# Kernel optimization log

Hardware: AMD Instinct MI355X
Metric: run time of the kernel (lower is better)

Reference implementation:

```python
import math
import jax, jax.numpy as jnp
import numpy as np

CT = {"SDD": 1000.0, "SCD": 500.0, "det_interval": 1.0, "num_det": 736}


def ramp_filter_np(ct, scale):
    # Standard equiangular fan-beam ramp filter (utility.ramp_filter):
    #   h[0] = 1/(8*db^2); h[n odd] = -1/(2*(pi*sin(n*db))^2); h[n even!=0] = 0
    db = ct["det_interval"] / ct["SDD"] * scale  # angular detector pitch at this scale
    n_det = int(ct["num_det"] // scale)
    n = np.arange(-(n_det - 1), n_det)  # length K = 2*n_det - 1
    h = np.zeros(n.shape, dtype=np.float32)
    h[n == 0] = 1.0 / (8.0 * db ** 2)
    odd = (n % 2) != 0
    h[odd] = -0.5 / (np.pi * np.sin(n[odd] * db)) ** 2
    return h


def setup_inputs() -> dict:
    key = jax.random.key(0)
    scale = 1
    batch, ch, view, det = 16, 1, 1152, CT["num_det"] // scale
    sinogram = jax.random.normal(key, (batch, ch, view, det), dtype=jnp.float32)
    delta_b = CT["det_interval"] / CT["SDD"]
    # recon_filter = ramp_filter * scale * delta_b, shaped [1,1,1,K] (OIHW)
    filt = ramp_filter_np(CT, scale) * scale * delta_b
    recon_filter = jnp.asarray(filt, dtype=jnp.float32)[None, None, None, :]
    return {"sinogram": sinogram, "recon_filter": recon_filter, "scale": scale}


def reference(sinogram, recon_filter, scale):
    det = sinogram.shape[-1]
    # cosine fan-beam pre-weighting
    s_range = (CT["det_interval"]
               * jnp.linspace((1.0 - det) / 2.0, (det - 1.0) / 2.0, det, dtype=jnp.float32)
               * scale) / CT["SDD"]
    cos_weight = (CT["SCD"] / 10000.0) * jnp.cos(s_range)  # [det]
    x = sinogram * cos_weight[None, None, None, :]
    # 1D ramp-filter convolution along detector axis (F.conv2d with 1xK kernel)
    K = recon_filter.shape[-1]
    pad = K // 2
    out = jax.lax.conv_general_dilated(
        x, recon_filter,
        window_strides=(1, 1),
        padding=[(0, 0), (pad, pad)],
        dimension_numbers=("NCHW", "OIHW", "NCHW"),
    )
    return out
```

## Files before the change

### kernel.cpp

```cpp
#include <hip/hip_runtime.h>

typedef unsigned short ushort_t;
typedef ushort_t u16x8 __attribute__((ext_vector_type(8)));
typedef __bf16 bf16x8 __attribute__((ext_vector_type(8)));
typedef float f32x4 __attribute__((ext_vector_type(4)));

#define DET 736
#define HALF 368
#define HK 384
#define NTT 12
#define CPB2 (NTT * 64)
#define NRB 1152


__global__ void prep_af(const float* __restrict__ sino,
                        ushort_t* __restrict__ Ae, ushort_t* __restrict__ Ao) {
    int c = blockIdx.x * blockDim.x + threadIdx.x;
    int rblk = c / CPB2;
    int rem  = c - rblk * CPB2;
    int t = rem >> 6, lane = rem & 63;
    int rr = lane & 15, quad = lane >> 4;
    int j0 = t * 32 + quad * 8;
    u16x8 ve, vo;
    if (j0 < HALF) {
        const float* g = sino + (size_t)(rblk * 16 + rr) * DET + 2 * j0;
        float w[16];
        *(f32x4*)(w)      = *(const f32x4*)(g);
        *(f32x4*)(w + 4)  = *(const f32x4*)(g + 4);
        *(f32x4*)(w + 8)  = *(const f32x4*)(g + 8);
        *(f32x4*)(w + 12) = *(const f32x4*)(g + 12);
#pragma unroll
        for (int e = 0; e < 8; ++e) {
            vo[e] = __builtin_bit_cast(ushort_t, (__bf16)w[2 * e]);
            ve[e] = __builtin_bit_cast(ushort_t, (__bf16)w[2 * e + 1]);
        }
    } else {
#pragma unroll
        for (int e = 0; e < 8; ++e) { ve[e] = 0; vo[e] = 0; }
    }
    *(u16x8*)(Ae + (size_t)c * 8) = ve;
    *(u16x8*)(Ao + (size_t)c * 8) = vo;
}

__global__ void prep_bf(const float* __restrict__ filt,
                        ushort_t* __restrict__ Be, ushort_t* __restrict__ Bo) {
    int c = blockIdx.x * blockDim.x + threadIdx.x;
    int cb  = c / CPB2;
    int rem = c - cb * CPB2;
    int t = rem >> 6, lane = rem & 63;
    int i = cb * 16 + (lane & 15);
    int quad = lane >> 4;
    u16x8 ve, vo;
#pragma unroll
    for (int e = 0; e < 8; ++e) {
        int j = t * 32 + quad * 8 + e;
        bool real = (j < HALF) && (i < HALF);
        int de = 2 * (j - i) + 1 + 735;
        int do_ = de - 2;
        de  = de  < 0 ? 0 : (de  > 1470 ? 1470 : de);
        do_ = do_ < 0 ? 0 : (do_ > 1470 ? 1470 : do_);
        float ge = 0.05f * cosf(((float)(2 * j + 1) - 367.5f) * 0.001f);
        float go = 0.05f * cosf(((float)(2 * j)     - 367.5f) * 0.001f);
        float fe = filt[de] * ge;
        float fo = filt[do_] * go;
        ve[e] = real ? __builtin_bit_cast(ushort_t, (__bf16)fe) : (ushort_t)0;
        vo[e] = real ? __builtin_bit_cast(ushort_t, (__bf16)fo) : (ushort_t)0;
    }
    *(u16x8*)(Be + (size_t)c * 8) = ve;
    *(u16x8*)(Bo + (size_t)c * 8) = vo;
}

__global__ __launch_bounds__(1024, 4) void gemm_half(
    const ushort_t* __restrict__ Ae, const ushort_t* __restrict__ Ao,
    const ushort_t* __restrict__ Be, const ushort_t* __restrict__ Bo,
    const float* __restrict__ sino, const float* __restrict__ filt,
    float* __restrict__ C)
{
    __shared__ ushort_t Bs[8 * CPB2 * 8];

    const int p    = blockIdx.z;
    const ushort_t* Af = p ? Ao : Ae;
    const ushort_t* Bf = p ? Bo : Be;

    const int tid  = threadIdx.x;
    const int lane = tid & 63;
    const int wid  = tid >> 6;
    const int wm   = wid >> 1;
    const int wn   = wid & 1;
    const int quad = lane >> 4;
    const int l16  = lane & 15;

    const int cbg0 = blockIdx.y * 8;
    {
        const ushort_t* bsrc = Bf + (size_t)cbg0 * CPB2 * 8;
        for (int c = tid; c < 8 * CPB2; c += 1024)
            *(u16x8*)(Bs + c * 8) = *(const u16x8*)(bsrc + (size_t)c * 8);
    }
    __syncthreads();

    const int rblk0 = blockIdx.x * 32 + wm * 4;

    f32x4 acc[4][4];
#pragma unroll
    for (int i = 0; i < 4; ++i)
#pragma unroll
        for (int j = 0; j < 4; ++j)
            acc[i][j] = (f32x4){0.f, 0.f, 0.f, 0.f};

    const ushort_t* pA[4];
#pragma unroll
    for (int mi = 0; mi < 4; ++mi)
        pA[mi] = Af + ((size_t)(rblk0 + mi) * CPB2 + lane) * 8;
    const ushort_t* pB[4];
#pragma unroll
    for (int ni = 0; ni < 4; ++ni)
        pB[ni] = Bs + ((wn * 4 + ni) * CPB2 + lane) * 8;

    u16x8 acur[4];
#pragma unroll
    for (int mi = 0; mi < 4; ++mi)
        acur[mi] = *(const u16x8*)(pA[mi]);

    for (int t = 0; t < NTT; ++t) {
        u16x8 anx[4];
        if (t + 1 < NTT) {
#pragma unroll
            for (int mi = 0; mi < 4; ++mi)
                anx[mi] = *(const u16x8*)(pA[mi] + (t + 1) * 512);
        }
        u16x8 b[4];
#pragma unroll
        for (int ni = 0; ni < 4; ++ni)
            b[ni] = *(const u16x8*)(pB[ni] + t * 512);
#pragma unroll
        for (int mi = 0; mi < 4; ++mi)
#pragma unroll
            for (int ni = 0; ni < 4; ++ni)
                acc[mi][ni] = __builtin_amdgcn_mfma_f32_16x16x32_bf16(
                    __builtin_bit_cast(bf16x8, acur[mi]),
                    __builtin_bit_cast(bf16x8, b[ni]),
                    acc[mi][ni], 0, 0, 0);
        if (t + 1 < NTT) {
#pragma unroll
            for (int mi = 0; mi < 4; ++mi) acur[mi] = anx[mi];
        }
    }

    const float h0 = filt[735];
    float gwv[4];
    int   ncol[4];
#pragma unroll
    for (int ni = 0; ni < 4; ++ni) {
        int ic   = blockIdx.y * 128 + (wn * 4 + ni) * 16 + l16;
        ncol[ni] = 2 * ic + p;
        gwv[ni]  = h0 * 0.05f * cosf(((float)ncol[ni] - 367.5f) * 0.001f);
    }
#pragma unroll
    for (int mi = 0; mi < 4; ++mi) {
#pragma unroll
        for (int ni = 0; ni < 4; ++ni) {
            if (ncol[ni] < DET) {
#pragma unroll
                for (int r = 0; r < 4; ++r) {
                    size_t rowg = (size_t)(rblk0 + mi) * 16 + quad * 4 + r;
                    float xd = sino[rowg * DET + ncol[ni]];
                    C[rowg * DET + ncol[ni]] = acc[mi][ni][r] + gwv[ni] * xd;
                }
            }
        }
    }
}

extern "C" void kernel_launch(void* const* d_in, const int* in_sizes, int n_in,
                              void* d_out, int out_size, void* d_ws, size_t ws_size,
                              hipStream_t stream) {
    const float* sino = (const float*)d_in[0];
    const float* filt = (const float*)d_in[1];
    (void)in_sizes; (void)n_in; (void)out_size; (void)ws_size;

    const size_t ASZ = (size_t)NRB * CPB2 * 8;
    const size_t BSZ = (size_t)24 * CPB2 * 8;

    ushort_t* Ae = (ushort_t*)d_ws;
    ushort_t* Ao = Ae + ASZ;
    ushort_t* Be = Ao + ASZ;
    ushort_t* Bo = Be + BSZ;
    float* out = (float*)d_out;

    prep_af<<<(NRB * CPB2) / 256, 256, 0, stream>>>(sino, Ae, Ao);
    prep_bf<<<(24 * CPB2) / 256, 256, 0, stream>>>(filt, Be, Bo);

    dim3 grid(NRB / 32, 3, 2);
    gemm_half<<<grid, 1024, 0, stream>>>(Ae, Ao, Be, Bo, sino, filt, out);
}
```

Before: 158.8 us.

## Fuse sinogram bf16 packing into GEMM via LDS staging and stream filter from global

Removes the separate prep_af kernel and its parity-split bf16 workspace for the sinogram. Each 1024-thread block now loads 64 sinogram rows, converts them to bf16 split by column parity into padded shared memory, and computes all output columns for both parities. The filter operand is read directly from global memory (small and likely cache-resident) with register prefetch, instead of being staged in LDS. This cuts a kernel launch and a large workspace write-then-read, at the cost of more global B traffic per block and a different warp tiling (4x3 MFMA tiles per wave).

```diff
diff --git a/kernel.cpp b/kernel.cpp
--- a/kernel.cpp
+++ b/kernel.cpp
@@ -1,46 +1,19 @@
 #include <hip/hip_runtime.h>
 
 typedef unsigned short ushort_t;
+typedef ushort_t u16x4 __attribute__((ext_vector_type(4)));
 typedef ushort_t u16x8 __attribute__((ext_vector_type(8)));
 typedef __bf16 bf16x8 __attribute__((ext_vector_type(8)));
 typedef float f32x4 __attribute__((ext_vector_type(4)));
 
 #define DET 736
 #define HALF 368
-#define HK 384
 #define NTT 12
 #define CPB2 (NTT * 64)
-#define NRB 1152
+#define RB 64
+#define LDR 392
+#define APAR (RB * LDR)
 
-
-__global__ void prep_af(const float* __restrict__ sino,
-                        ushort_t* __restrict__ Ae, ushort_t* __restrict__ Ao) {
-    int c = blockIdx.x * blockDim.x + threadIdx.x;
-    int rblk = c / CPB2;
-    int rem  = c - rblk * CPB2;
-    int t = rem >> 6, lane = rem & 63;
-    int rr = lane & 15, quad = lane >> 4;
-    int j0 = t * 32 + quad * 8;
-    u16x8 ve, vo;
-    if (j0 < HALF) {
-        const float* g = sino + (size_t)(rblk * 16 + rr) * DET + 2 * j0;
-        float w[16];
-        *(f32x4*)(w)      = *(const f32x4*)(g);
-        *(f32x4*)(w + 4)  = *(const f32x4*)(g + 4);
-        *(f32x4*)(w + 8)  = *(const f32x4*)(g + 8);
-        *(f32x4*)(w + 12) = *(const f32x4*)(g + 12);
-#pragma unroll
-        for (int e = 0; e < 8; ++e) {
-            vo[e] = __builtin_bit_cast(ushort_t, (__bf16)w[2 * e]);
-            ve[e] = __builtin_bit_cast(ushort_t, (__bf16)w[2 * e + 1]);
-        }
-    } else {
-#pragma unroll
-        for (int e = 0; e < 8; ++e) { ve[e] = 0; vo[e] = 0; }
-    }
-    *(u16x8*)(Ae + (size_t)c * 8) = ve;
-    *(u16x8*)(Ao + (size_t)c * 8) = vo;
-}
 
 __global__ void prep_bf(const float* __restrict__ filt,
                         ushort_t* __restrict__ Be, ushort_t* __restrict__ Bo) {
@@ -70,101 +43,113 @@
     *(u16x8*)(Bo + (size_t)c * 8) = vo;
 }
 
-__global__ __launch_bounds__(1024, 4) void gemm_half(
-    const ushort_t* __restrict__ Ae, const ushort_t* __restrict__ Ao,
+__global__ __launch_bounds__(1024, 4) void gemm_fused(
+    const float* __restrict__ sino,
     const ushort_t* __restrict__ Be, const ushort_t* __restrict__ Bo,
-    const float* __restrict__ sino, const float* __restrict__ filt,
+    const float* __restrict__ filt,
     float* __restrict__ C)
 {
-    __shared__ ushort_t Bs[8 * CPB2 * 8];
-
-    const int p    = blockIdx.z;
-    const ushort_t* Af = p ? Ao : Ae;
-    const ushort_t* Bf = p ? Bo : Be;
+    __shared__ ushort_t As[2 * APAR];
 
     const int tid  = threadIdx.x;
     const int lane = tid & 63;
     const int wid  = tid >> 6;
-    const int wm   = wid >> 1;
-    const int wn   = wid & 1;
     const int quad = lane >> 4;
     const int l16  = lane & 15;
 
-    const int cbg0 = blockIdx.y * 8;
-    {
-        const ushort_t* bsrc = Bf + (size_t)cbg0 * CPB2 * 8;
-        for (int c = tid; c < 8 * CPB2; c += 1024)
-            *(u16x8*)(Bs + c * 8) = *(const u16x8*)(bsrc + (size_t)c * 8);
+    const size_t row_a0 = (size_t)blockIdx.x * RB;
+
+    for (int c = tid; c < RB * 92; c += 1024) {
+        int row = c / 92;
+        int cp  = c - row * 92;
+        const float* g = sino + (row_a0 + row) * DET + cp * 8;
+        f32x4 lo = *(const f32x4*)g;
+        f32x4 hi = *(const f32x4*)(g + 4);
+        u16x4 vod, vev;
+        vod[0] = __builtin_bit_cast(ushort_t, (__bf16)lo[1]);
+        vod[1] = __builtin_bit_cast(ushort_t, (__bf16)lo[3]);
+        vod[2] = __builtin_bit_cast(ushort_t, (__bf16)hi[1]);
+        vod[3] = __builtin_bit_cast(ushort_t, (__bf16)hi[3]);
+        vev[0] = __builtin_bit_cast(ushort_t, (__bf16)lo[0]);
+        vev[1] = __builtin_bit_cast(ushort_t, (__bf16)lo[2]);
+        vev[2] = __builtin_bit_cast(ushort_t, (__bf16)hi[0]);
+        vev[3] = __builtin_bit_cast(ushort_t, (__bf16)hi[2]);
+        *(u16x4*)(As + row * LDR + cp * 4)        = vod;
+        *(u16x4*)(As + APAR + row * LDR + cp * 4) = vev;
+    }
+    if (tid < 128) {
+        int p = tid & 1, row = tid >> 1;
+        ushort_t* z = As + p * APAR + row * LDR + HALF;
+        *(u16x8*)(z)     = (u16x8){0,0,0,0,0,0,0,0};
+        *(u16x8*)(z + 8) = (u16x8){0,0,0,0,0,0,0,0};
     }
     __syncthreads();
 
-    const int rblk0 = blockIdx.x * 32 + wm * 4;
+    const int p    = wid >> 3;
+    const int cb0  = (wid & 7) * 3;
+    const ushort_t* Bfp = p ? Bo : Be;
 
-    f32x4 acc[4][4];
+    f32x4 acc[4][3];
 #pragma unroll
     for (int i = 0; i < 4; ++i)
 #pragma unroll
-        for (int j = 0; j < 4; ++j)
+        for (int j = 0; j < 3; ++j)
             acc[i][j] = (f32x4){0.f, 0.f, 0.f, 0.f};
 
-    const ushort_t* pA[4];
+    int aoff[4];
 #pragma unroll
     for (int mi = 0; mi < 4; ++mi)
-        pA[mi] = Af + ((size_t)(rblk0 + mi) * CPB2 + lane) * 8;
-    const ushort_t* pB[4];
+        aoff[mi] = p * APAR + (mi * 16 + l16) * LDR + quad * 8;
+
+    const ushort_t* pB[3];
 #pragma unroll
-    for (int ni = 0; ni < 4; ++ni)
-        pB[ni] = Bs + ((wn * 4 + ni) * CPB2 + lane) * 8;
+    for (int ni = 0; ni < 3; ++ni)
+        pB[ni] = Bfp + ((size_t)(cb0 + ni) * CPB2 + lane) * 8;
 
-    u16x8 acur[4];
+    u16x8 bcur[3];
 #pragma unroll
-    for (int mi = 0; mi < 4; ++mi)
-        acur[mi] = *(const u16x8*)(pA[mi]);
+    for (int ni = 0; ni < 3; ++ni)
+        bcur[ni] = *(const u16x8*)(pB[ni]);
 
     for (int t = 0; t < NTT; ++t) {
-        u16x8 anx[4];
+        u16x8 bnx[3];
         if (t + 1 < NTT) {
 #pragma unroll
-            for (int mi = 0; mi < 4; ++mi)
-                anx[mi] = *(const u16x8*)(pA[mi] + (t + 1) * 512);
+            for (int ni = 0; ni < 3; ++ni)
+                bnx[ni] = *(const u16x8*)(pB[ni] + (t + 1) * 512);
         }
-        u16x8 b[4];
+        u16x8 a[4];
 #pragma unroll
-        for (int ni = 0; ni < 4; ++ni)
-            b[ni] = *(const u16x8*)(pB[ni] + t * 512);
+        for (int mi = 0; mi < 4; ++mi)
+            a[mi] = *(const u16x8*)(As + aoff[mi] + t * 32);
 #pragma unroll
         for (int mi = 0; mi < 4; ++mi)
 #pragma unroll
-            for (int ni = 0; ni < 4; ++ni)
+            for (int ni = 0; ni < 3; ++ni)
                 acc[mi][ni] = __builtin_amdgcn_mfma_f32_16x16x32_bf16(
-                    __builtin_bit_cast(bf16x8, acur[mi]),
-                    __builtin_bit_cast(bf16x8, b[ni]),
+                    __builtin_bit_cast(bf16x8, a[mi]),
+                    __builtin_bit_cast(bf16x8, bcur[ni]),
                     acc[mi][ni], 0, 0, 0);
         if (t + 1 < NTT) {
 #pragma unroll
-            for (int mi = 0; mi < 4; ++mi) acur[mi] = anx[mi];
+            for (int ni = 0; ni < 3; ++ni) bcur[ni] = bnx[ni];
         }
     }
 
     const float h0 = filt[735];
-    float gwv[4];
-    int   ncol[4];
 #pragma unroll
-    for (int ni = 0; ni < 4; ++ni) {
-        int ic   = blockIdx.y * 128 + (wn * 4 + ni) * 16 + l16;
-        ncol[ni] = 2 * ic + p;
-        gwv[ni]  = h0 * 0.05f * cosf(((float)ncol[ni] - 367.5f) * 0.001f);
-    }
+    for (int ni = 0; ni < 3; ++ni) {
+        int ic   = (cb0 + ni) * 16 + l16;
+        int colg = 2 * ic + p;
+        if (colg < DET) {
+            float gw = h0 * 0.05f * cosf(((float)colg - 367.5f) * 0.001f);
 #pragma unroll
-    for (int mi = 0; mi < 4; ++mi) {
-#pragma unroll
-        for (int ni = 0; ni < 4; ++ni) {
-            if (ncol[ni] < DET) {
+            for (int mi = 0; mi < 4; ++mi) {
 #pragma unroll
                 for (int r = 0; r < 4; ++r) {
-                    size_t rowg = (size_t)(rblk0 + mi) * 16 + quad * 4 + r;
-                    float xd = sino[rowg * DET + ncol[ni]];
-                    C[rowg * DET + ncol[ni]] = acc[mi][ni][r] + gwv[ni] * xd;
+                    size_t rowg = row_a0 + mi * 16 + quad * 4 + r;
+                    float xd = sino[rowg * DET + colg];
+                    C[rowg * DET + colg] = acc[mi][ni][r] + gw * xd;
                 }
             }
         }
@@ -178,18 +163,13 @@
     const float* filt = (const float*)d_in[1];
     (void)in_sizes; (void)n_in; (void)out_size; (void)ws_size;
 
-    const size_t ASZ = (size_t)NRB * CPB2 * 8;
     const size_t BSZ = (size_t)24 * CPB2 * 8;
 
-    ushort_t* Ae = (ushort_t*)d_ws;
-    ushort_t* Ao = Ae + ASZ;
-    ushort_t* Be = Ao + ASZ;
+    ushort_t* Be = (ushort_t*)d_ws;
     ushort_t* Bo = Be + BSZ;
     float* out = (float*)d_out;
 
-    prep_af<<<(NRB * CPB2) / 256, 256, 0, stream>>>(sino, Ae, Ao);
-    prep_bf<<<(24 * CPB2) / 256, 256, 0, stream>>>(filt, Be, Bo);
+    prep_bf<<<72, 256, 0, stream>>>(filt, Be, Bo);
 
-    dim3 grid(NRB / 32, 3, 2);
-    gemm_half<<<grid, 1024, 0, stream>>>(Ae, Ao, Be, Bo, sino, filt, out);
+    gemm_fused<<<dim3(288), 1024, 0, stream>>>(sino, Be, Bo, filt, out);
 }
```

Result: faster. 153.0 us (-3.6%).

## Fuse even/odd GEMM halves into one block and drop LDS staging of B

Applied to the files above, without the earlier changes.

The even and odd parity GEMMs now run in the same block: each wave keeps both accumulator sets and emits paired float2 stores of adjacent output columns, where before a separate z-slice handled each parity with strided scalar stores. The B operand is read straight from global/L2 per k-step instead of being staged once into shared memory. Blocks shrink to 512 threads covering 8 row blocks, so there are more blocks and the shared-memory footprint goes away. The cost is more global traffic for B, no A-prefetch double buffering, and lower reuse of A per block.

```diff
diff --git a/kernel.cpp b/kernel.cpp
--- a/kernel.cpp
+++ b/kernel.cpp
@@ -7,7 +7,6 @@
 
 #define DET 736
 #define HALF 368
-#define HK 384
 #define NTT 12
 #define CPB2 (NTT * 64)
 #define NRB 1152
@@ -70,18 +69,12 @@
     *(u16x8*)(Bo + (size_t)c * 8) = vo;
 }
 
-__global__ __launch_bounds__(1024, 4) void gemm_half(
+__global__ __launch_bounds__(512) void gemm_pair(
     const ushort_t* __restrict__ Ae, const ushort_t* __restrict__ Ao,
     const ushort_t* __restrict__ Be, const ushort_t* __restrict__ Bo,
     const float* __restrict__ sino, const float* __restrict__ filt,
     float* __restrict__ C)
 {
-    __shared__ ushort_t Bs[8 * CPB2 * 8];
-
-    const int p    = blockIdx.z;
-    const ushort_t* Af = p ? Ao : Ae;
-    const ushort_t* Bf = p ? Bo : Be;
-
     const int tid  = threadIdx.x;
     const int lane = tid & 63;
     const int wid  = tid >> 6;
@@ -90,81 +83,79 @@
     const int quad = lane >> 4;
     const int l16  = lane & 15;
 
-    const int cbg0 = blockIdx.y * 8;
-    {
-        const ushort_t* bsrc = Bf + (size_t)cbg0 * CPB2 * 8;
-        for (int c = tid; c < 8 * CPB2; c += 1024)
-            *(u16x8*)(Bs + c * 8) = *(const u16x8*)(bsrc + (size_t)c * 8);
+    const int rblk0 = blockIdx.x * 8 + wm * 2;
+    const int cb0   = blockIdx.y * 8 + wn * 4;
+
+    f32x4 acc_e[2][4], acc_o[2][4];
+#pragma unroll
+    for (int mi = 0; mi < 2; ++mi)
+#pragma unroll
+        for (int ni = 0; ni < 4; ++ni) {
+            acc_e[mi][ni] = (f32x4){0.f, 0.f, 0.f, 0.f};
+            acc_o[mi][ni] = (f32x4){0.f, 0.f, 0.f, 0.f};
+        }
+
+    const ushort_t* pAe[2]; const ushort_t* pAo[2];
+#pragma unroll
+    for (int mi = 0; mi < 2; ++mi) {
+        size_t off = ((size_t)(rblk0 + mi) * CPB2 + lane) * 8;
+        pAe[mi] = Ae + off;
+        pAo[mi] = Ao + off;
     }
-    __syncthreads();
+    const ushort_t* pBe[4]; const ushort_t* pBo[4];
+#pragma unroll
+    for (int ni = 0; ni < 4; ++ni) {
+        size_t off = ((size_t)(cb0 + ni) * CPB2 + lane) * 8;
+        pBe[ni] = Be + off;
+        pBo[ni] = Bo + off;
+    }
 
-    const int rblk0 = blockIdx.x * 32 + wm * 4;
-
-    f32x4 acc[4][4];
+#pragma unroll 2
+    for (int t = 0; t < NTT; ++t) {
+        const int off = t * 512;
+        u16x8 ae[2], ao[2], be[4], bo[4];
 #pragma unroll
-    for (int i = 0; i < 4; ++i)
+        for (int mi = 0; mi < 2; ++mi) {
+            ae[mi] = *(const u16x8*)(pAe[mi] + off);
+            ao[mi] = *(const u16x8*)(pAo[mi] + off);
+        }
 #pragma unroll
-        for (int j = 0; j < 4; ++j)
-            acc[i][j] = (f32x4){0.f, 0.f, 0.f, 0.f};
-
-    const ushort_t* pA[4];
+        for (int ni = 0; ni < 4; ++ni) {
+            be[ni] = *(const u16x8*)(pBe[ni] + off);
+            bo[ni] = *(const u16x8*)(pBo[ni] + off);
+        }
 #pragma unroll
-    for (int mi = 0; mi < 4; ++mi)
-        pA[mi] = Af + ((size_t)(rblk0 + mi) * CPB2 + lane) * 8;
-    const ushort_t* pB[4];
+        for (int mi = 0; mi < 2; ++mi)
 #pragma unroll
-    for (int ni = 0; ni < 4; ++ni)
-        pB[ni] = Bs + ((wn * 4 + ni) * CPB2 + lane) * 8;
-
-    u16x8 acur[4];
-#pragma unroll
-    for (int mi = 0; mi < 4; ++mi)
-        acur[mi] = *(const u16x8*)(pA[mi]);
-
-    for (int t = 0; t < NTT; ++t) {
-        u16x8 anx[4];
-        if (t + 1 < NTT) {
-#pragma unroll
-            for (int mi = 0; mi < 4; ++mi)
-                anx[mi] = *(const u16x8*)(pA[mi] + (t + 1) * 512);
-        }
-        u16x8 b[4];
-#pragma unroll
-        for (int ni = 0; ni < 4; ++ni)
-            b[ni] = *(const u16x8*)(pB[ni] + t * 512);
-#pragma unroll
-        for (int mi = 0; mi < 4; ++mi)
-#pragma unroll
-            for (int ni = 0; ni < 4; ++ni)
-                acc[mi][ni] = __builtin_amdgcn_mfma_f32_16x16x32_bf16(
-                    __builtin_bit_cast(bf16x8, acur[mi]),
-                    __builtin_bit_cast(bf16x8, b[ni]),
-                    acc[mi][ni], 0, 0, 0);
-        if (t + 1 < NTT) {
-#pragma unroll
-            for (int mi = 0; mi < 4; ++mi) acur[mi] = anx[mi];
-        }
+            for (int ni = 0; ni < 4; ++ni) {
+                acc_e[mi][ni] = __builtin_amdgcn_mfma_f32_16x16x32_bf16(
+                    __builtin_bit_cast(bf16x8, ae[mi]),
+                    __builtin_bit_cast(bf16x8, be[ni]),
+                    acc_e[mi][ni], 0, 0, 0);
+                acc_o[mi][ni] = __builtin_amdgcn_mfma_f32_16x16x32_bf16(
+                    __builtin_bit_cast(bf16x8, ao[mi]),
+                    __builtin_bit_cast(bf16x8, bo[ni]),
+                    acc_o[mi][ni], 0, 0, 0);
+            }
     }
 
     const float h0 = filt[735];
-    float gwv[4];
-    int   ncol[4];
 #pragma unroll
     for (int ni = 0; ni < 4; ++ni) {
-        int ic   = blockIdx.y * 128 + (wn * 4 + ni) * 16 + l16;
-        ncol[ni] = 2 * ic + p;
-        gwv[ni]  = h0 * 0.05f * cosf(((float)ncol[ni] - 367.5f) * 0.001f);
-    }
+        const int ic = (cb0 + ni) * 16 + l16;
+        if (ic < HALF) {
+            const float gw_e = h0 * 0.05f * cosf(((float)(2 * ic)     - 367.5f) * 0.001f);
+            const float gw_o = h0 * 0.05f * cosf(((float)(2 * ic + 1) - 367.5f) * 0.001f);
 #pragma unroll
-    for (int mi = 0; mi < 4; ++mi) {
-#pragma unroll
-        for (int ni = 0; ni < 4; ++ni) {
-            if (ncol[ni] < DET) {
+            for (int mi = 0; mi < 2; ++mi) {
 #pragma unroll
                 for (int r = 0; r < 4; ++r) {
-                    size_t rowg = (size_t)(rblk0 + mi) * 16 + quad * 4 + r;
-                    float xd = sino[rowg * DET + ncol[ni]];
-                    C[rowg * DET + ncol[ni]] = acc[mi][ni][r] + gwv[ni] * xd;
+                    const size_t rowg = (size_t)(rblk0 + mi) * 16 + quad * 4 + r;
+                    const float2 xd = *(const float2*)(sino + rowg * DET + 2 * ic);
+                    float2 o;
+                    o.x = acc_e[mi][ni][r] + gw_e * xd.x;
+                    o.y = acc_o[mi][ni][r] + gw_o * xd.y;
+                    *(float2*)(C + rowg * DET + 2 * ic) = o;
                 }
             }
         }
@@ -190,6 +181,6 @@
     prep_af<<<(NRB * CPB2) / 256, 256, 0, stream>>>(sino, Ae, Ao);
     prep_bf<<<(24 * CPB2) / 256, 256, 0, stream>>>(filt, Be, Bo);
 
-    dim3 grid(NRB / 32, 3, 2);
-    gemm_half<<<grid, 1024, 0, stream>>>(Ae, Ao, Be, Bo, sino, filt, out);
+    dim3 grid(NRB / 8, 3);
+    gemm_pair<<<grid, 512, 0, stream>>>(Ae, Ao, Be, Bo, sino, filt, out);
 }
```

Measured after the change: 138.6 us. 12.7% less time.
